# Optimization experiments

Hardware: AMD Instinct MI355X
Metric: run time of the kernel (lower is better)

Reference implementation:

```python
import jax, jax.numpy as jnp
import numpy as np

N = 4096
M = 1024
APPERTURE = 250
L1, L2, L3, PRED = 1024, 512, 128, 1
EPS = 1e-6


def _layer_norm(x, gamma, beta):
    # torch x.std(-1) is unbiased (ddof=1)
    mean = jnp.mean(x, axis=-1, keepdims=True)
    std = jnp.std(x, axis=-1, ddof=1, keepdims=True)
    return gamma * (x - mean) / (std + EPS) + beta


def _self_attention(x, Wq, Wk, Wv, Wo, band_mask):
    # x: [n, m]; Linear(bias=False) => x @ W.T
    K = x @ Wk.T
    Q = (x @ Wq.T) * 0.06
    V = x @ Wv.T
    logits = Q @ K.T                      # [n, n]
    logits = jnp.where(band_mask, logits, -jnp.inf)  # keep |i-j| < apperture
    att = jax.nn.softmax(logits, axis=-1)
    # original: y = (V^T @ att)^T == att^T @ V  (note the transpose!)
    y = att.T @ V
    return y @ Wo.T, att


def setup_inputs() -> dict:
    key = jax.random.key(0)
    ks = jax.random.split(key, 20)
    s = 0.02
    inp = {
        'x1': jax.random.normal(ks[0], (1, N, M), jnp.float32),
        'x2': jax.random.normal(ks[1], (1, N, M), jnp.float32),
        'x3': jax.random.normal(ks[2], (1, N, M), jnp.float32),
        'Wq': jax.random.normal(ks[3], (M, M), jnp.float32) * s,
        'Wk': jax.random.normal(ks[4], (M, M), jnp.float32) * s,
        'Wv': jax.random.normal(ks[5], (M, M), jnp.float32) * s,
        'Wo': jax.random.normal(ks[6], (M, M), jnp.float32) * s,
        'ka_w': jax.random.normal(ks[7], (L1, M), jnp.float32) * s,
        'ka_b': jnp.zeros((L1,), jnp.float32),
        'kb_w': jax.random.normal(ks[8], (L2, L1), jnp.float32) * s,
        'kb_b': jnp.zeros((L2,), jnp.float32),
        'kc_w': jax.random.normal(ks[9], (L3, L2), jnp.float32) * s,
        'kc_b': jnp.zeros((L3,), jnp.float32),
        'kd_w': jax.random.normal(ks[10], (PRED, L3), jnp.float32) * s,
        'kd_b': jnp.zeros((PRED,), jnp.float32),
        'g13': jnp.ones((M,), jnp.float32),
        'b13': jnp.zeros((M,), jnp.float32),
        'gkc': jnp.ones((L3,), jnp.float32),
        'bkc': jnp.zeros((L3,), jnp.float32),
        'seq_len': N,
    }
    return inp


def reference(x1, x2, x3, Wq, Wk, Wv, Wo, ka_w, ka_b, kb_w, kb_b, kc_w, kc_b,
              kd_w, kd_b, g13, b13, gkc, bkc, seq_len):
    x1 = x1.reshape(-1, x1.shape[2])
    x2 = x2.reshape(-1, x2.shape[2])
    x3 = x3.reshape(-1, x3.shape[2])
    n = x1.shape[0]
    idx = jnp.arange(n)
    band_mask = jnp.abs(idx[:, None] - idx[None, :]) < APPERTURE  # allowed

    y1, att1 = _self_attention(x1, Wq, Wk, Wv, Wo, band_mask)
    y2, _ = _self_attention(x2, Wq, Wk, Wv, Wo, band_mask)
    y3, _ = _self_attention(x3, Wq, Wk, Wv, Wo, band_mask)

    # residual + (dropout == identity in eval) + shared LayerNorm
    y1 = _layer_norm(y1 + x1, g13, b13)
    y2 = _layer_norm(y2 + x2, g13, b13)
    y3 = _layer_norm(y3 + x3, g13, b13)

    y = y1 + y2 + y3  # cmb == [1,1,1]
    y = y @ ka_w.T + ka_b
    y = y @ kb_w.T + kb_b
    y = jax.nn.relu(y @ kc_w.T + kc_b)
    y = _layer_norm(y, gkc, bkc)
    y = jax.nn.sigmoid(y @ kd_w.T + kd_b)
    return y.reshape(1, -1), att1
```

## Files before the change

kernel.cpp:

```cpp
#include <hip/hip_runtime.h>
#include <hip/hip_bf16.h>
#include <cstdint>
#include <cstddef>

#define NSEQ 4096
#define MDIM 1024

typedef __attribute__((ext_vector_type(8))) short short8;
typedef __attribute__((ext_vector_type(4))) float f32x4;
typedef __attribute__((ext_vector_type(2))) long long2v;
typedef __attribute__((ext_vector_type(8))) int int8v;
typedef __attribute__((ext_vector_type(4))) int int4v;

typedef const __attribute__((address_space(1))) void gvoid_t;
typedef __attribute__((address_space(3))) void lvoid_t;

__device__ __forceinline__ unsigned short f2b(float x) {
  union { float f; unsigned int u; } a; a.f = x;
  unsigned int r = (a.u + 0x7fffu + ((a.u >> 16) & 1u)) >> 16;
  return (unsigned short)r;
}
__device__ __forceinline__ float b2f(unsigned short u) {
  union { float f; unsigned int u32; } a; a.u32 = ((unsigned int)u) << 16;
  return a.f;
}
__device__ __forceinline__ unsigned char f2e4(float x) {
  return (unsigned char)(__builtin_amdgcn_cvt_pk_fp8_f32(x, x, 0, false) & 0xff);
}
__device__ __forceinline__ unsigned int f2e4x4(float a, float b, float c, float d) {
  unsigned int lo = __builtin_amdgcn_cvt_pk_fp8_f32(a, b, 0, false);
  return (unsigned int)__builtin_amdgcn_cvt_pk_fp8_f32(c, d, lo, true);
}

__device__ __forceinline__ int8v pack32(const unsigned char* p0,
                                        const unsigned char* p1) {
  int4v lo = *(const int4v*)p0;
  int4v hi = *(const int4v*)p1;
  int8v r;
  r[0] = lo[0]; r[1] = lo[1]; r[2] = lo[2]; r[3] = lo[3];
  r[4] = hi[0]; r[5] = hi[1]; r[6] = hi[2]; r[7] = hi[3];
  return r;
}

__global__ __launch_bounds__(256) void k_cvt_all(
    const float* __restrict__ s0, const float* __restrict__ s1,
    const float* __restrict__ s2, const float* __restrict__ s3,
    const float* __restrict__ s4, const float* __restrict__ s5,
    const float* __restrict__ s6,
    const float* __restrict__ xa, const float* __restrict__ xb,
    const float* __restrict__ xc,
    unsigned char* __restrict__ Wf8, unsigned short* __restrict__ Wmlp,
    unsigned char* __restrict__ Xdst, float* __restrict__ sums) {
  int idx = blockIdx.x * 256 + threadIdx.x;
  if (idx < 1048576) {
    int seg = idx >> 18, local = idx & 262143;
    const float* src = (seg == 0) ? s0 : (seg == 1) ? s1 : (seg == 2) ? s2 : s3;
    float4 v = *(const float4*)(src + (size_t)local * 4);
    *(unsigned int*)(Wf8 + (size_t)idx * 4) =
        f2e4x4(v.x * 64.f, v.y * 64.f, v.z * 64.f, v.w * 64.f);
  } else if (idx < 1458176) {
    int i2 = idx - 1048576;
    const float* src; int local;
    if (i2 < 262144) { src = s4; local = i2; }
    else if (i2 < 393216) { src = s5; local = i2 - 262144; }
    else { src = s6; local = i2 - 393216; }
    float4 v = *(const float4*)(src + (size_t)local * 4);
    ushort4 o; o.x = f2b(v.x); o.y = f2b(v.y); o.z = f2b(v.z); o.w = f2b(v.w);
    *(ushort4*)(Wmlp + (size_t)i2 * 4) = o;
  } else if (idx < 4603904) {
    int i2 = idx - 1458176;
    int seg = i2 >> 20, local = i2 & 1048575;
    const float* src = (seg == 0) ? xa : (seg == 1) ? xb : xc;
    float4 v = *(const float4*)(src + (size_t)local * 4);
    *(unsigned int*)(Xdst + (size_t)i2 * 4) = f2e4x4(v.x, v.y, v.z, v.w);
  } else {
    int i3 = idx - 4603904;
    *(float4*)(sums + (size_t)i3 * 4) = make_float4(0.f, 0.f, 0.f, 0.f);
  }
}

template <int MODE, int OKIND, int DO_EXP>
__device__ __forceinline__ void gemm_core(
    const unsigned char* __restrict__ A, int lda,
    const unsigned char* __restrict__ B, int ldb,
    void* __restrict__ Cout, void* __restrict__ Cout2, int ldc,
    int K, float alpha,
    const unsigned char* __restrict__ A1, const unsigned char* __restrict__ A2,
    float* __restrict__ sums_out, unsigned char* __restrict__ smem) {
  int bx = blockIdx.x, by = blockIdx.y;
  const unsigned char* Ab;
  const unsigned char* Bb;
  void* Cdst = Cout;
  int k0 = 0, k1 = K, b_koff = 0;
  int ldce = ldc;
  int rbase, cbase;
  int ldae = lda, ldbe = ldb;
  if constexpr (MODE == 0) {
    Ab = A + (size_t)by * 128 * lda;
    Bb = B + (size_t)bx * 128 * ldb;
    rbase = bx * 128; cbase = by * 128;
  } else if constexpr (MODE == 3) {
    if (by < 16) {
      Ab = A + (size_t)by * 128 * lda;
      Bb = B + (size_t)bx * 128 * ldb;
      if (by >= 8) Cdst = Cout2;
      rbase = bx * 128; cbase = (by & 7) * 128;
    } else {
      Ab = B + (size_t)bx * 128 * ldb;
      Bb = A1 + (size_t)(by - 16) * 128 * 1024;
      Cdst = (void*)const_cast<unsigned char*>(A2);
      rbase = (by - 16) * 128; cbase = bx * 128;
      ldce = 3 * NSEQ;
    }
  } else if constexpr (MODE == 1) {
    int s = bx >> 5, ti = bx & 31;
    int bt = ti + by - 2;
    Ab = A + (size_t)(s * 32 + bt) * 128 * lda;
    Bb = B + (size_t)bx * 128 * ldb;
    rbase = bx * 128; cbase = by * 128;
  } else {
    int s = bx >> 5, ti = bx & 31;
    Ab = A + (size_t)by * 128 * lda + s * NSEQ;
    const unsigned char* Bbase = (s == 0) ? B : ((s == 1) ? A1 : A2);
    Bb = Bbase + (size_t)ti * 128 * 640;
    ldbe = 640;
    int lo = ti - 2; if (lo < 0) lo = 0;
    int hi = ti + 3; if (hi > 32) hi = 32;
    k0 = lo * 128; k1 = hi * 128;
    b_koff = (ti - 2) * 128;
    rbase = bx * 128; cbase = by * 128;
  }

  const int t = threadIdx.x;
  const int l = t & 63;
  const int w = t >> 6;
  const int fr = l & 15;
  const int quad = l >> 4;
  const int wm = (w >> 1) * 64;
  const int wn = (w & 1) * 64;
  const int fq4 = quad * 4;

  int srow[4], scg[4], sloff[4];
#pragma unroll
  for (int j = 0; j < 4; j++) {
    srow[j] = w * 32 + j * 8 + (l >> 3);
    scg[j] = ((l & 7) - srow[j]) & 7;
    sloff[j] = (w * 32 + j * 8) * 128 + l * 16;
  }

  f32x4 acc[4][4];
#pragma unroll
  for (int m = 0; m < 4; m++)
#pragma unroll
    for (int n = 0; n < 4; n++) acc[m][n] = (f32x4){0.f, 0.f, 0.f, 0.f};

  const int c0 = quad * 2;
  const int nt = (k1 - k0) >> 7;

  {
    int kk = k0, kb = kk - b_koff;
#pragma unroll
    for (int j = 0; j < 4; j++)
      __builtin_amdgcn_global_load_lds(
          (gvoid_t*)(Ab + (size_t)srow[j] * ldae + kk + scg[j] * 16),
          (lvoid_t*)(smem + sloff[j]), 16, 0, 0);
#pragma unroll
    for (int j = 0; j < 4; j++)
      __builtin_amdgcn_global_load_lds(
          (gvoid_t*)(Bb + (size_t)srow[j] * ldbe + kb + scg[j] * 16),
          (lvoid_t*)(smem + 16384 + sloff[j]), 16, 0, 0);
  }

  for (int tt = 0; tt < nt; tt++) {
    if (tt + 1 < nt) {
      int kk = k0 + (tt + 1) * 128, kb = kk - b_koff;
      unsigned char* Asn = smem + ((tt + 1) & 1) * 32768;
#pragma unroll
      for (int j = 0; j < 4; j++)
        __builtin_amdgcn_global_load_lds(
            (gvoid_t*)(Ab + (size_t)srow[j] * ldae + kk + scg[j] * 16),
            (lvoid_t*)(Asn + sloff[j]), 16, 0, 0);
#pragma unroll
      for (int j = 0; j < 4; j++)
        __builtin_amdgcn_global_load_lds(
            (gvoid_t*)(Bb + (size_t)srow[j] * ldbe + kb + scg[j] * 16),
            (lvoid_t*)(Asn + 16384 + sloff[j]), 16, 0, 0);
      __builtin_amdgcn_sched_barrier(0);
      asm volatile("s_waitcnt vmcnt(8)" ::: "memory");
    } else {
      asm volatile("s_waitcnt vmcnt(0)" ::: "memory");
    }
    asm volatile("s_barrier" ::: "memory");

    const unsigned char* Asc = smem + (tt & 1) * 32768;
    const unsigned char* Bsc = Asc + 16384;
    int8v a8[4], b8[4];
#pragma unroll
    for (int m = 0; m < 4; m++) {
      int r = wm + m * 16 + fr;
      int s0i = (c0 + r) & 7, s1i = (s0i + 1) & 7;
      a8[m] = pack32(Asc + r * 128 + s0i * 16, Asc + r * 128 + s1i * 16);
    }
#pragma unroll
    for (int n = 0; n < 4; n++) {
      int r = wn + n * 16 + fr;
      int s0i = (c0 + r) & 7, s1i = (s0i + 1) & 7;
      b8[n] = pack32(Bsc + r * 128 + s0i * 16, Bsc + r * 128 + s1i * 16);
    }
#pragma unroll
    for (int m = 0; m < 4; m++)
#pragma unroll
      for (int n = 0; n < 4; n++)
        acc[m][n] = __builtin_amdgcn_mfma_scale_f32_16x16x128_f8f6f4(
            a8[m], b8[n], acc[m][n], 0, 0, 0, 0x7F7F7F7F, 0, 0x7F7F7F7F);
    asm volatile("s_barrier" ::: "memory");
  }

  float rowsum[4] = {0.f, 0.f, 0.f, 0.f};
  const int jb = ((bx & 31) - 2) * 128;
#pragma unroll
  for (int m = 0; m < 4; m++) {
#pragma unroll
    for (int n = 0; n < 4; n++) {
      int oc = cbase + wm + m * 16 + fq4;
      int orow = rbase + wn + n * 16 + fr;
      float v0 = acc[m][n][0] * alpha, v1 = acc[m][n][1] * alpha;
      float v2 = acc[m][n][2] * alpha, v3 = acc[m][n][3] * alpha;
      if constexpr (OKIND == 1) {
        if constexpr (DO_EXP) {
          v0 = __expf(v0); v1 = __expf(v1); v2 = __expf(v2); v3 = __expf(v3);
          if constexpr (MODE == 1) {
            int d0 = (orow & 4095) - (jb + oc);
            rowsum[n] += ((unsigned)(d0 + 249) < 499u ? v0 : 0.f)
                       + ((unsigned)(d0 + 248) < 499u ? v1 : 0.f)
                       + ((unsigned)(d0 + 247) < 499u ? v2 : 0.f)
                       + ((unsigned)(d0 + 246) < 499u ? v3 : 0.f);
          }
        }
        ushort4 o; o.x = f2b(v0); o.y = f2b(v1); o.z = f2b(v2); o.w = f2b(v3);
        *(uint2*)((unsigned short*)Cdst + (size_t)orow * ldce + oc) = *(uint2*)&o;
      } else {
        *(unsigned int*)((unsigned char*)Cdst + (size_t)orow * ldce + oc) =
            f2e4x4(v0, v1, v2, v3);
      }
    }
  }
  if constexpr (MODE == 1 && DO_EXP) {
#pragma unroll
    for (int n = 0; n < 4; n++) {
      float sv = rowsum[n];
      sv += __shfl_xor(sv, 16);
      sv += __shfl_xor(sv, 32);
      if (quad == 0) {
        int orow = rbase + wn + n * 16 + fr;
        atomicAdd(sums_out + orow, sv);
      }
    }
  }
}

__global__ __launch_bounds__(256) void k_qkv(
    const unsigned char* __restrict__ A, const unsigned char* __restrict__ B,
    void* __restrict__ Cout, void* __restrict__ Cout2, float alpha,
    const unsigned char* __restrict__ A1, const unsigned char* __restrict__ A2) {
  __shared__ unsigned char smem[4 * 128 * 128];
  gemm_core<3, 2, 0>(A, 1024, B, 1024, Cout, Cout2, 1024, 1024, alpha,
                     A1, A2, nullptr, smem);
}

__global__ __launch_bounds__(256) void k_logits(
    const unsigned char* __restrict__ A, const unsigned char* __restrict__ B,
    void* __restrict__ Cout, float alpha, float* __restrict__ sums) {
  int ti = blockIdx.x & 31;
  int bt = ti + (int)blockIdx.y - 2;
  if (bt < 0 || bt >= 32) return;
  __shared__ unsigned char smem[4 * 128 * 128];
  gemm_core<1, 1, 1>(A, 1024, B, 1024, Cout, nullptr, 640, 1024, alpha,
                     nullptr, nullptr, sums, smem);
}

__global__ __launch_bounds__(256) void k_av(
    const unsigned char* __restrict__ A, const unsigned char* __restrict__ B,
    void* __restrict__ Cout, float alpha,
    const unsigned char* __restrict__ A1, const unsigned char* __restrict__ A2) {
  __shared__ unsigned char smem[4 * 128 * 128];
  gemm_core<2, 2, 0>(A, 3 * NSEQ, B, 640, Cout, nullptr, 1024, NSEQ, alpha,
                     A1, A2, nullptr, smem);
}

__global__ __launch_bounds__(256) void k_wo(
    const unsigned char* __restrict__ A, const unsigned char* __restrict__ B,
    void* __restrict__ Cout, float alpha) {
  __shared__ unsigned char smem[4 * 128 * 128];
  gemm_core<0, 1, 0>(A, 1024, B, 1024, Cout, nullptr, 1024, 1024, alpha,
                     nullptr, nullptr, nullptr, smem);
}

__global__ __launch_bounds__(256) void k_gemm64(
    const unsigned short* __restrict__ A, int lda,
    const unsigned short* __restrict__ B, int ldb,
    void* __restrict__ Cout, int ldc, int K,
    const float* __restrict__ bias, int relu, int out_bf16) {
  __shared__ unsigned short smem[4 * 64 * 64];
  int bx = blockIdx.x, by = blockIdx.y;
  const unsigned short* Ab = A + (size_t)by * 64 * lda;
  const unsigned short* Bb = B + (size_t)bx * 64 * ldb;
  int rbase = bx * 64, cbase = by * 64;

  const int t = threadIdx.x;
  const int l = t & 63;
  const int w = t >> 6;
  const int fr = l & 15;
  const int quad = l >> 4;
  const int wm = (w & 1) * 32;
  const int wn = (w >> 1) * 32;
  const int fq4 = quad * 4;

  int srow[2], scg[2], sloff[2];
#pragma unroll
  for (int j = 0; j < 2; j++) {
    srow[j] = w * 16 + j * 8 + (l >> 3);
    scg[j] = ((l & 7) - srow[j]) & 7;
    sloff[j] = (w * 16 + j * 8) * 64 + l * 8;
  }

  f32x4 acc[2][2];
#pragma unroll
  for (int m = 0; m < 2; m++)
#pragma unroll
    for (int n = 0; n < 2; n++) acc[m][n] = (f32x4){0.f, 0.f, 0.f, 0.f};

  const int nt = K >> 6;

#pragma unroll
  for (int j = 0; j < 2; j++)
    __builtin_amdgcn_global_load_lds(
        (gvoid_t*)(Ab + (size_t)srow[j] * lda + scg[j] * 8),
        (lvoid_t*)(smem + sloff[j]), 16, 0, 0);
#pragma unroll
  for (int j = 0; j < 2; j++)
    __builtin_amdgcn_global_load_lds(
        (gvoid_t*)(Bb + (size_t)srow[j] * ldb + scg[j] * 8),
        (lvoid_t*)(smem + 4096 + sloff[j]), 16, 0, 0);

  for (int tt = 0; tt < nt; tt++) {
    __syncthreads();
    if (tt + 1 < nt) {
      int kk = (tt + 1) * 64;
      unsigned short* Asn = smem + ((tt + 1) & 1) * 8192;
#pragma unroll
      for (int j = 0; j < 2; j++)
        __builtin_amdgcn_global_load_lds(
            (gvoid_t*)(Ab + (size_t)srow[j] * lda + kk + scg[j] * 8),
            (lvoid_t*)(Asn + sloff[j]), 16, 0, 0);
#pragma unroll
      for (int j = 0; j < 2; j++)
        __builtin_amdgcn_global_load_lds(
            (gvoid_t*)(Bb + (size_t)srow[j] * ldb + kk + scg[j] * 8),
            (lvoid_t*)(Asn + 4096 + sloff[j]), 16, 0, 0);
    }
    const unsigned short* Asc = smem + (tt & 1) * 8192;
    const unsigned short* Bsc = Asc + 4096;
#pragma unroll
    for (int s = 0; s < 2; s++) {
      short8 af[2], bf[2];
#pragma unroll
      for (int m = 0; m < 2; m++) {
        int r = wm + m * 16 + fr;
        int slot = (s * 4 + quad + r) & 7;
        af[m] = *(const short8*)(Asc + r * 64 + slot * 8);
      }
#pragma unroll
      for (int n = 0; n < 2; n++) {
        int r = wn + n * 16 + fr;
        int slot = (s * 4 + quad + r) & 7;
        bf[n] = *(const short8*)(Bsc + r * 64 + slot * 8);
      }
#pragma unroll
      for (int m = 0; m < 2; m++)
#pragma unroll
        for (int n = 0; n < 2; n++)
          acc[m][n] = __builtin_amdgcn_mfma_f32_16x16x32_bf16(af[m], bf[n], acc[m][n], 0, 0, 0);
    }
  }

#pragma unroll
  for (int m = 0; m < 2; m++) {
#pragma unroll
    for (int n = 0; n < 2; n++) {
      int oc = cbase + wm + m * 16 + fq4;
      int orow = rbase + wn + n * 16 + fr;
      float4 bv = bias ? *(const float4*)(bias + oc) : make_float4(0.f, 0.f, 0.f, 0.f);
      float v0 = acc[m][n][0] + bv.x, v1 = acc[m][n][1] + bv.y;
      float v2 = acc[m][n][2] + bv.z, v3 = acc[m][n][3] + bv.w;
      if (relu) {
        v0 = fmaxf(v0, 0.f); v1 = fmaxf(v1, 0.f);
        v2 = fmaxf(v2, 0.f); v3 = fmaxf(v3, 0.f);
      }
      if (out_bf16) {
        ushort4 o; o.x = f2b(v0); o.y = f2b(v1); o.z = f2b(v2); o.w = f2b(v3);
        *(uint2*)((unsigned short*)Cout + (size_t)orow * ldc + oc) = *(uint2*)&o;
      } else {
        *(float4*)((float*)Cout + (size_t)orow * ldc + oc) = make_float4(v0, v1, v2, v3);
      }
    }
  }
}

__global__ __launch_bounds__(256) void k_build_attT(const unsigned short* __restrict__ Eband,
                                                    const float* __restrict__ sums,
                                                    unsigned char* __restrict__ t0,
                                                    unsigned char* __restrict__ t1,
                                                    unsigned char* __restrict__ t2) {
  int byy = blockIdx.y;
  int s = byy >> 5, ti = byy & 31;
  int tj = ti + (int)blockIdx.x - 2;
  if (tj < 0 || tj >= 32) return;
  unsigned char* dst = (s == 0) ? t0 : ((s == 1) ? t1 : t2);
  __shared__ unsigned char T[128][132];
  int t = threadIdx.x;
  int c0 = (ti - tj + 2) * 128;
  int colg = (t & 31) * 4;
  for (int jj = t >> 5; jj < 128; jj += 8) {
    int jg = s * NSEQ + tj * 128 + jj;
    float inv = 16.f / sums[jg];
    ushort4 v = *(const ushort4*)&Eband[(size_t)jg * 640 + c0 + colg];
    float vv[4] = {b2f(v.x), b2f(v.y), b2f(v.z), b2f(v.w)};
#pragma unroll
    for (int q = 0; q < 4; q++) {
      int i = ti * 128 + colg + q;
      int d = i - (tj * 128 + jj);
      float a = (d < 250 && d > -250) ? vv[q] * inv : 0.f;
      T[colg + q][jj] = f2e4(a);
    }
  }
  __syncthreads();
  int jb0 = (tj - ti + 2) * 128;
  for (int ii = t >> 5; ii < 128; ii += 8) {
    size_t o = (size_t)(ti * 128 + ii) * 640 + jb0 + colg;
    *(unsigned int*)(dst + o) = *(const unsigned int*)&T[ii][colg];
  }
}

__global__ __launch_bounds__(256) void k_write_att(const unsigned short* __restrict__ Eband,
                                                   const float* __restrict__ sums,
                                                   float* __restrict__ att) {
  int i = blockIdx.x;
  int ti = i >> 7, cbase = (ti - 2) * 128;
  int jlo = i - 249; if (jlo < 0) jlo = 0;
  int jhi = i + 249; if (jhi > NSEQ - 1) jhi = NSEQ - 1;
  float inv = 1.f / sums[i];
  const unsigned short* L = Eband + (size_t)i * 640;
  float* arow = att + (size_t)i * NSEQ;
  for (int j0 = threadIdx.x * 4; j0 < NSEQ; j0 += 1024) {
    float ov[4];
#pragma unroll
    for (int q = 0; q < 4; q++) {
      int j = j0 + q;
      ov[q] = (j >= jlo && j <= jhi) ? b2f(L[j - cbase]) * inv : 0.f;
    }
    *(float4*)(arow + j0) = make_float4(ov[0], ov[1], ov[2], ov[3]);
  }
}

__global__ __launch_bounds__(256) void k_ln3(const unsigned short* __restrict__ yo,
                                             const float* __restrict__ x1,
                                             const float* __restrict__ x2,
                                             const float* __restrict__ x3,
                                             const float* __restrict__ g,
                                             const float* __restrict__ b,
                                             unsigned short* __restrict__ ysum_b) {
  int i = blockIdx.x, t = threadIdx.x;
  int w = t >> 6, lane = t & 63;
  __shared__ float red[8];
  const float* xs[3] = {x1, x2, x3};
  float4 gg = *(const float4*)(g + t * 4);
  float4 bb = *(const float4*)(b + t * 4);
  float acc[4] = {0.f, 0.f, 0.f, 0.f};
  for (int s = 0; s < 3; s++) {
    ushort4 yv = *(const ushort4*)(yo + ((size_t)(s * NSEQ + i)) * MDIM + t * 4);
    float4 xx = *(const float4*)(xs[s] + (size_t)i * MDIM + t * 4);
    float v[4] = {b2f(yv.x) + xx.x, b2f(yv.y) + xx.y, b2f(yv.z) + xx.z, b2f(yv.w) + xx.w};
    float s1 = v[0] + v[1] + v[2] + v[3];
    float s2 = v[0]*v[0] + v[1]*v[1] + v[2]*v[2] + v[3]*v[3];
    for (int off = 32; off; off >>= 1) { s1 += __shfl_xor(s1, off); s2 += __shfl_xor(s2, off); }
    __syncthreads();
    if (lane == 0) { red[w] = s1; red[4 + w] = s2; }
    __syncthreads();
    float S1 = red[0] + red[1] + red[2] + red[3];
    float S2 = red[4] + red[5] + red[6] + red[7];
    float mean = S1 * (1.f / 1024.f);
    float var = (S2 - S1 * mean) * (1.f / 1023.f);
    float rstd = 1.f / (sqrtf(var) + 1e-6f);
    acc[0] += gg.x * (v[0] - mean) * rstd + bb.x;
    acc[1] += gg.y * (v[1] - mean) * rstd + bb.y;
    acc[2] += gg.z * (v[2] - mean) * rstd + bb.z;
    acc[3] += gg.w * (v[3] - mean) * rstd + bb.w;
  }
  ushort4 o;
  o.x = f2b(acc[0]); o.y = f2b(acc[1]); o.z = f2b(acc[2]); o.w = f2b(acc[3]);
  *(ushort4*)(ysum_b + (size_t)i * MDIM + t * 4) = o;
}

__global__ __launch_bounds__(128) void k_final(const float* __restrict__ h3,
                                               const float* __restrict__ g,
                                               const float* __restrict__ b,
                                               const float* __restrict__ kdw,
                                               const float* __restrict__ kdb,
                                               float* __restrict__ yout) {
  int i = blockIdx.x, t = threadIdx.x;
  float v = h3[(size_t)i * 128 + t];
  float s1 = v, s2 = v * v;
  for (int off = 32; off; off >>= 1) { s1 += __shfl_xor(s1, off); s2 += __shfl_xor(s2, off); }
  __shared__ float red[4];
  int w = t >> 6, lane = t & 63;
  if (lane == 0) { red[w] = s1; red[2 + w] = s2; }
  __syncthreads();
  float S1 = red[0] + red[1], S2 = red[2] + red[3];
  float mean = S1 * (1.f / 128.f);
  float var = (S2 - S1 * mean) * (1.f / 127.f);
  float rstd = 1.f / (sqrtf(var) + 1e-6f);
  float ln = g[t] * (v - mean) * rstd + b[t];
  float p = ln * kdw[t];
  for (int off = 32; off; off >>= 1) p += __shfl_xor(p, off);
  __syncthreads();
  if (lane == 0) red[w] = p;
  __syncthreads();
  if (t == 0) {
    float z = red[0] + red[1] + kdb[0];
    yout[i] = 1.f / (1.f + __expf(-z));
  }
}

extern "C" void kernel_launch(void* const* d_in, const int* in_sizes, int n_in,
                              void* d_out, int out_size, void* d_ws, size_t ws_size,
                              hipStream_t stream) {
  const float* x1 = (const float*)d_in[0];
  const float* x2 = (const float*)d_in[1];
  const float* x3 = (const float*)d_in[2];
  const float* Wq = (const float*)d_in[3];
  const float* Wk = (const float*)d_in[4];
  const float* Wv = (const float*)d_in[5];
  const float* Wo = (const float*)d_in[6];
  const float* ka_w = (const float*)d_in[7];
  const float* ka_b = (const float*)d_in[8];
  const float* kb_w = (const float*)d_in[9];
  const float* kb_b = (const float*)d_in[10];
  const float* kc_w = (const float*)d_in[11];
  const float* kc_b = (const float*)d_in[12];
  const float* kd_w = (const float*)d_in[13];
  const float* kd_b = (const float*)d_in[14];
  const float* g13 = (const float*)d_in[15];
  const float* b13 = (const float*)d_in[16];
  const float* gkc = (const float*)d_in[17];
  const float* bkc = (const float*)d_in[18];

  float* y_out = (float*)d_out;
  float* att_out = y_out + NSEQ;

  char* ws = (char*)d_ws;
  size_t off = 0;
  auto alloc = [&](size_t bytes) -> void* {
    void* p = ws + off;
    off += (bytes + 255) & ~(size_t)255;
    return p;
  };
  const size_t NM = (size_t)3 * NSEQ * MDIM;
  unsigned char* Wf = (unsigned char*)alloc(4 * 1048576);
  unsigned short* Wmlp = (unsigned short*)alloc((1048576 + 524288 + 65536) * 2);
  unsigned char* Xf = (unsigned char*)alloc(NM);
  unsigned char* Qf = (unsigned char*)alloc(NM);
  unsigned char* Kf = (unsigned char*)alloc(NM);
  unsigned char* VTf = (unsigned char*)alloc(NM);
  unsigned short* Eband = (unsigned short*)alloc((size_t)3 * NSEQ * 640 * 2);
  float* sums = (float*)alloc((size_t)3 * NSEQ * 4);
  unsigned char* aT0 = (unsigned char*)alloc((size_t)NSEQ * 640);
  unsigned char* aT1 = (unsigned char*)alloc((size_t)NSEQ * 640);
  unsigned char* aT2 = (unsigned char*)alloc((size_t)NSEQ * 640);
  unsigned char* Wv_f = Wf + 2097152;
  unsigned char* Wo_f = Wf + 3145728;
  unsigned short* ka_b16 = Wmlp;
  unsigned short* kb_b16 = Wmlp + 1048576;
  unsigned short* kc_b16 = Wmlp + 1572864;
  unsigned char* yb = Xf;
  unsigned short* yo = (unsigned short*)Qf;
  unsigned short* ysum_b = (unsigned short*)VTf;
  unsigned short* h1b = (unsigned short*)Xf;
  unsigned short* h2b = (unsigned short*)Qf;
  float* h3 = (float*)aT0;

  k_cvt_all<<<17996, 256, 0, stream>>>(Wq, Wk, Wv, Wo, ka_w, kb_w, kc_w,
                                       x1, x2, x3, Wf, Wmlp, Xf, sums);

  k_qkv<<<dim3(96, 24), 256, 0, stream>>>(Wf, Xf, Qf, Kf, 1.f / 64.f, Wv_f, VTf);
  k_logits<<<dim3(96, 5), 256, 0, stream>>>(Kf, Qf, Eband, 0.06f, sums);
  k_build_attT<<<dim3(5, 96), 256, 0, stream>>>(Eband, sums, aT0, aT1, aT2);
  k_av<<<dim3(96, 8), 256, 0, stream>>>(VTf, aT0, yb, 0.5f, aT1, aT2);
  k_write_att<<<4096, 256, 0, stream>>>(Eband, sums, att_out);
  k_wo<<<dim3(96, 8), 256, 0, stream>>>(Wo_f, yb, yo, 1.f / 512.f);
  k_ln3<<<4096, 256, 0, stream>>>(yo, x1, x2, x3, g13, b13, ysum_b);

  k_gemm64<<<dim3(64, 16), 256, 0, stream>>>(ka_b16, 1024, ysum_b, 1024, h1b, 1024,
                                             1024, ka_b, 0, 1);
  k_gemm64<<<dim3(64, 8), 256, 0, stream>>>(kb_b16, 1024, h1b, 1024, h2b, 512,
                                            1024, kb_b, 0, 1);
  k_gemm64<<<dim3(64, 2), 256, 0, stream>>>(kc_b16, 512, h2b, 512, h3, 128,
                                            512, kc_b, 1, 0);
  k_final<<<4096, 128, 0, stream>>>(h3, gkc, bkc, kd_w, kd_b, y_out);
}
```

Baseline: 325.3 us.

## Load A operand directly from global into registers, stage only B in LDS

The FP8 GEMM core stops staging the A tile through LDS. Each wave now reads its A fragments straight from global memory into registers at the start of every k-step, while B stays double-buffered in LDS. LDS per block is halved (64KB to 32KB), which could allow more resident blocks and removes the A LDS write/read traffic. In exchange, A loads are issued without prefetch, so their global latency is exposed on each iteration. Rows shared between waves are also fetched redundantly, leaning on cache.

```diff
diff --git a/kernel.cpp b/kernel.cpp
--- a/kernel.cpp
+++ b/kernel.cpp
@@ -148,6 +148,8 @@
     sloff[j] = (w * 32 + j * 8) * 128 + l * 16;
   }
 
+  const unsigned char* Al = Ab + (size_t)(wm + fr) * ldae + quad * 32;
+
   f32x4 acc[4][4];
 #pragma unroll
   for (int m = 0; m < 4; m++)
@@ -158,49 +160,39 @@
   const int nt = (k1 - k0) >> 7;
 
   {
-    int kk = k0, kb = kk - b_koff;
-#pragma unroll
-    for (int j = 0; j < 4; j++)
-      __builtin_amdgcn_global_load_lds(
-          (gvoid_t*)(Ab + (size_t)srow[j] * ldae + kk + scg[j] * 16),
-          (lvoid_t*)(smem + sloff[j]), 16, 0, 0);
+    int kb = k0 - b_koff;
 #pragma unroll
     for (int j = 0; j < 4; j++)
       __builtin_amdgcn_global_load_lds(
           (gvoid_t*)(Bb + (size_t)srow[j] * ldbe + kb + scg[j] * 16),
-          (lvoid_t*)(smem + 16384 + sloff[j]), 16, 0, 0);
+          (lvoid_t*)(smem + sloff[j]), 16, 0, 0);
   }
 
   for (int tt = 0; tt < nt; tt++) {
+    int kk = k0 + tt * 128;
+    int8v a8[4];
+#pragma unroll
+    for (int m = 0; m < 4; m++) {
+      const unsigned char* p = Al + (size_t)(m * 16) * ldae + kk;
+      a8[m] = pack32(p, p + 16);
+    }
     if (tt + 1 < nt) {
-      int kk = k0 + (tt + 1) * 128, kb = kk - b_koff;
-      unsigned char* Asn = smem + ((tt + 1) & 1) * 32768;
-#pragma unroll
-      for (int j = 0; j < 4; j++)
-        __builtin_amdgcn_global_load_lds(
-            (gvoid_t*)(Ab + (size_t)srow[j] * ldae + kk + scg[j] * 16),
-            (lvoid_t*)(Asn + sloff[j]), 16, 0, 0);
+      int kb = kk + 128 - b_koff;
+      unsigned char* Bn = smem + ((tt + 1) & 1) * 16384;
 #pragma unroll
       for (int j = 0; j < 4; j++)
         __builtin_amdgcn_global_load_lds(
             (gvoid_t*)(Bb + (size_t)srow[j] * ldbe + kb + scg[j] * 16),
-            (lvoid_t*)(Asn + 16384 + sloff[j]), 16, 0, 0);
+            (lvoid_t*)(Bn + sloff[j]), 16, 0, 0);
       __builtin_amdgcn_sched_barrier(0);
+      asm volatile("s_waitcnt vmcnt(12)" ::: "memory");
+    } else {
       asm volatile("s_waitcnt vmcnt(8)" ::: "memory");
-    } else {
-      asm volatile("s_waitcnt vmcnt(0)" ::: "memory");
     }
     asm volatile("s_barrier" ::: "memory");
 
-    const unsigned char* Asc = smem + (tt & 1) * 32768;
-    const unsigned char* Bsc = Asc + 16384;
-    int8v a8[4], b8[4];
-#pragma unroll
-    for (int m = 0; m < 4; m++) {
-      int r = wm + m * 16 + fr;
-      int s0i = (c0 + r) & 7, s1i = (s0i + 1) & 7;
-      a8[m] = pack32(Asc + r * 128 + s0i * 16, Asc + r * 128 + s1i * 16);
-    }
+    const unsigned char* Bsc = smem + (tt & 1) * 16384;
+    int8v b8[4];
 #pragma unroll
     for (int n = 0; n < 4; n++) {
       int r = wn + n * 16 + fr;
@@ -263,7 +255,7 @@
     const unsigned char* __restrict__ A, const unsigned char* __restrict__ B,
     void* __restrict__ Cout, void* __restrict__ Cout2, float alpha,
     const unsigned char* __restrict__ A1, const unsigned char* __restrict__ A2) {
-  __shared__ unsigned char smem[4 * 128 * 128];
+  __shared__ unsigned char smem[2 * 128 * 128];
   gemm_core<3, 2, 0>(A, 1024, B, 1024, Cout, Cout2, 1024, 1024, alpha,
                      A1, A2, nullptr, smem);
 }
@@ -274,7 +266,7 @@
   int ti = blockIdx.x & 31;
   int bt = ti + (int)blockIdx.y - 2;
   if (bt < 0 || bt >= 32) return;
-  __shared__ unsigned char smem[4 * 128 * 128];
+  __shared__ unsigned char smem[2 * 128 * 128];
   gemm_core<1, 1, 1>(A, 1024, B, 1024, Cout, nullptr, 640, 1024, alpha,
                      nullptr, nullptr, sums, smem);
 }
@@ -283,7 +275,7 @@
     const unsigned char* __restrict__ A, const unsigned char* __restrict__ B,
     void* __restrict__ Cout, float alpha,
     const unsigned char* __restrict__ A1, const unsigned char* __restrict__ A2) {
-  __shared__ unsigned char smem[4 * 128 * 128];
+  __shared__ unsigned char smem[2 * 128 * 128];
   gemm_core<2, 2, 0>(A, 3 * NSEQ, B, 640, Cout, nullptr, 1024, NSEQ, alpha,
                      A1, A2, nullptr, smem);
 }
@@ -291,7 +283,7 @@
 __global__ __launch_bounds__(256) void k_wo(
     const unsigned char* __restrict__ A, const unsigned char* __restrict__ B,
     void* __restrict__ Cout, float alpha) {
-  __shared__ unsigned char smem[4 * 128 * 128];
+  __shared__ unsigned char smem[2 * 128 * 128];
   gemm_core<0, 1, 0>(A, 1024, B, 1024, Cout, nullptr, 1024, 1024, alpha,
                      nullptr, nullptr, nullptr, smem);
 }
```

New measurement: 390.6 us. +20.1%, slower.
